# Optimization experiments

Measured on AMD Instinct MI355X. Metric: run time of the kernel, lower is better.

## Reference

```python
import jax, jax.numpy as jnp
import numpy as np


def setup_inputs() -> dict:
    key = jax.random.key(0)
    ka, kb = jax.random.split(key)
    B, S, I, J = 8, 8192, 256, 256
    a = jax.random.normal(ka, (B, S, I), dtype=jnp.float32)
    b = jax.random.normal(kb, (B, S, J), dtype=jnp.float32)
    return {"a": a, "b": b}


def reference(a, b):
    # mean_s(a_si outer b_sj) == (a^T @ b) / s, without materializing [*, i, j, s]
    s = a.shape[-2]
    out = jnp.einsum('...si,...sj->...ij', a, b) / s  # [*, i, j]
    return out
```

## Files before the change

kernel.cpp:

```cpp
#include <hip/hip_runtime.h>

typedef __bf16 bf16x8 __attribute__((ext_vector_type(8)));
typedef float f32x16 __attribute__((ext_vector_type(16)));
typedef float f32x4 __attribute__((ext_vector_type(4)));

#define S_TOTAL 8192
#define DIM 256
#define BK 16
#define NSP 16

__global__ __launch_bounds__(512, 4) void opm_partial(
    const float* __restrict__ A, const float* __restrict__ Bm,
    __bf16* __restrict__ dstbf, float* __restrict__ dstf32,
    int nsp, int kc, float scale)
{
    __shared__ float lA[3][BK * 256];
    __shared__ float lB[3][BK * 64];

    const int tid = threadIdx.x;
    const int w   = tid >> 6;
    const int l   = tid & 63;

    const int bid = blockIdx.x;
    const int x   = bid & 7;
    const int s   = bid >> 3;
    const int jq  = s & 3;
    const int gx  = s >> 2;
    const int g   = gx * 8 + x;
    const int batch = g / nsp;
    const int sp    = g % nsp;

    const long long base = (long long)batch * S_TOTAL * DIM;
    const int s0 = sp * kc;
    const int wr = w >> 1, wc = w & 1;
    const int lane31 = l & 31;
    const int hi = l >> 5;
    const int niter = kc / BK;

    f32x16 acc[2] = {};

    auto issue = [&](int it) {
        const int b3 = it % 3;
        const long long sb = (long long)(s0 + it * BK);
        __builtin_amdgcn_global_load_lds(
            (const __attribute__((address_space(1))) unsigned int*)(A + base + (sb + w) * DIM + 4 * l),
            (__attribute__((address_space(3))) unsigned int*)&lA[b3][w * 256], 16, 0, 0);
        __builtin_amdgcn_global_load_lds(
            (const __attribute__((address_space(1))) unsigned int*)(A + base + (sb + w + 8) * DIM + 4 * l),
            (__attribute__((address_space(3))) unsigned int*)&lA[b3][(w + 8) * 256], 16, 0, 0);
        if (w < 4) {
            __builtin_amdgcn_global_load_lds(
                (const __attribute__((address_space(1))) unsigned int*)(Bm + base + (sb + 4 * w + (l >> 4)) * DIM + jq * 64 + 4 * (l & 15)),
                (__attribute__((address_space(3))) unsigned int*)&lB[b3][4 * w * 64], 16, 0, 0);
        }
    };

    auto compute = [&](int b3) {
        const int i0 = wr * 64 + lane31;
        const int j0 = wc * 32 + lane31;
        bf16x8 af[2], bfv;
        #pragma unroll
        for (int mi = 0; mi < 2; ++mi)
            #pragma unroll
            for (int e = 0; e < 8; ++e)
                af[mi][e] = (__bf16)lA[b3][(hi * 8 + e) * 256 + i0 + mi * 32];
        #pragma unroll
        for (int e = 0; e < 8; ++e)
            bfv[e] = (__bf16)lB[b3][(hi * 8 + e) * 64 + j0];
        acc[0] = __builtin_amdgcn_mfma_f32_32x32x16_bf16(af[0], bfv, acc[0], 0, 0, 0);
        acc[1] = __builtin_amdgcn_mfma_f32_32x32x16_bf16(af[1], bfv, acc[1], 0, 0, 0);
    };

    issue(0);
    issue(1);

    for (int it = 0; it < niter; ++it) {
        const int rem = niter - 1 - it;
        if (w < 4) {
            if (rem >= 1) asm volatile("s_waitcnt vmcnt(3)" ::: "memory");
            else          asm volatile("s_waitcnt vmcnt(0)" ::: "memory");
        } else {
            if (rem >= 1) asm volatile("s_waitcnt vmcnt(2)" ::: "memory");
            else          asm volatile("s_waitcnt vmcnt(0)" ::: "memory");
        }
        __builtin_amdgcn_s_barrier();
        if (it + 2 < niter) issue(it + 2);
        compute(it % 3);
    }

    if (dstf32) {
        float* o = dstf32 + (long long)batch * (256 * 256) + jq * 64;
        #pragma unroll
        for (int mi = 0; mi < 2; ++mi)
        #pragma unroll
        for (int q = 0; q < 16; ++q) {
            const int row = (q & 3) + 8 * (q >> 2) + 4 * hi;
            const int i = wr * 64 + mi * 32 + row;
            const int j = wc * 32 + lane31;
            o[i * 256 + j] = acc[mi][q] * scale;
        }
    } else {
        __bf16* o = dstbf + (long long)((batch * nsp + sp) * 4 + jq) * 16384;
        __bf16* ebuf = (__bf16*)&lA[0][0];
        #pragma unroll
        for (int band = 0; band < 2; ++band) {
            __syncthreads();
            if ((wr >> 1) == band) {
                #pragma unroll
                for (int mi = 0; mi < 2; ++mi)
                #pragma unroll
                for (int q = 0; q < 16; ++q) {
                    const int lr = (wr & 1) * 64 + mi * 32 + (q & 3) + 8 * (q >> 2) + 4 * hi;
                    ebuf[lr * 64 + wc * 32 + lane31] = (__bf16)(acc[mi][q] * scale);
                }
            }
            __syncthreads();
            #pragma unroll
            for (int h = 0; h < 2; ++h) {
                const int G = tid + h * 512;
                *(bf16x8*)&o[band * 8192 + G * 8] = *(const bf16x8*)&ebuf[G * 8];
            }
        }
    }
}

__global__ __launch_bounds__(256) void opm_reduce16(
    const __bf16* __restrict__ ws, float* __restrict__ out)
{
    const int idx = blockIdx.x * 256 + threadIdx.x;
    const int batch = idx >> 13;
    const int gg  = idx & 8191;
    const int i   = gg >> 5;
    const int jgc = gg & 31;
    const int jq  = jgc >> 3;
    const int c8  = (jgc & 7) * 8;

    const bf16x8* p = (const bf16x8*)(ws + ((long long)(batch * NSP) * 4 + jq) * 16384 + i * 64 + c8);
    bf16x8 v[NSP];
    #pragma unroll
    for (int sp = 0; sp < NSP; ++sp) v[sp] = p[sp * 8192];

    float sacc[8] = {0.f, 0.f, 0.f, 0.f, 0.f, 0.f, 0.f, 0.f};
    #pragma unroll
    for (int sp = 0; sp < NSP; ++sp)
        #pragma unroll
        for (int e = 0; e < 8; ++e) sacc[e] += (float)v[sp][e];

    f32x4 lo = { sacc[0], sacc[1], sacc[2], sacc[3] };
    f32x4 hiv = { sacc[4], sacc[5], sacc[6], sacc[7] };
    lo  *= (1.0f / 8192.0f);
    hiv *= (1.0f / 8192.0f);
    ((f32x4*)out)[idx * 2]     = lo;
    ((f32x4*)out)[idx * 2 + 1] = hiv;
}

extern "C" void kernel_launch(void* const* d_in, const int* in_sizes, int n_in,
                              void* d_out, int out_size, void* d_ws, size_t ws_size,
                              hipStream_t stream)
{
    (void)in_sizes; (void)n_in; (void)out_size;
    const float* A  = (const float*)d_in[0];
    const float* Bm = (const float*)d_in[1];
    float* out = (float*)d_out;

    if (ws_size >= (size_t)8 * NSP * 4 * 16384 * sizeof(__bf16)) {
        opm_partial<<<32 * NSP, 512, 0, stream>>>(A, Bm, (__bf16*)d_ws, nullptr,
                                                  NSP, S_TOTAL / NSP, 1.0f);
        opm_reduce16<<<256, 256, 0, stream>>>((const __bf16*)d_ws, out);
    } else {
        opm_partial<<<32, 512, 0, stream>>>(A, Bm, nullptr, out, 1, S_TOTAL, 1.0f / 8192.0f);
    }
}
```

Before: 41.53 us.

## Switch partial GEMM tiles from 256x64 strips to 128x128 quadrants

Each block now computes a 128x128 quadrant of the output instead of a 256x64 column strip. It loads half of A's columns and half of B's columns per s-row, which cuts per-block global loads and removes redundant A reads across j-quarter blocks. Every wave now issues equal load counts, which simplifies the waitcnt logic, and LDS use shrinks. The workspace layout and reduce-kernel indexing are updated to match the quadrant ordering.

New measurement: 34.04 us. 1.22x faster.

```diff
diff --git a/kernel.cpp b/kernel.cpp
--- a/kernel.cpp
+++ b/kernel.cpp
@@ -14,25 +14,26 @@
     __bf16* __restrict__ dstbf, float* __restrict__ dstf32,
     int nsp, int kc, float scale)
 {
-    __shared__ float lA[3][BK * 256];
-    __shared__ float lB[3][BK * 64];
+    __shared__ float lds[3 * 4096];
 
     const int tid = threadIdx.x;
     const int w   = tid >> 6;
     const int l   = tid & 63;
 
-    const int bid = blockIdx.x;
-    const int x   = bid & 7;
-    const int s   = bid >> 3;
-    const int jq  = s & 3;
-    const int gx  = s >> 2;
-    const int g   = gx * 8 + x;
+    const int bid  = blockIdx.x;
+    const int x    = bid & 7;
+    const int r    = bid >> 3;
+    const int mate = r & 3;
+    const int gx   = r >> 2;
+    const int ih   = mate >> 1;
+    const int jh   = mate & 1;
+    const int g    = gx * 8 + x;
     const int batch = g / nsp;
     const int sp    = g % nsp;
 
     const long long base = (long long)batch * S_TOTAL * DIM;
     const int s0 = sp * kc;
-    const int wr = w >> 1, wc = w & 1;
+    const int wr = w >> 2, wc = w & 3;
     const int lane31 = l & 31;
     const int hi = l >> 5;
     const int niter = kc / BK;
@@ -40,33 +41,28 @@
     f32x16 acc[2] = {};
 
     auto issue = [&](int it) {
-        const int b3 = it % 3;
-        const long long sb = (long long)(s0 + it * BK);
+        float* buf = &lds[(it % 3) * 4096];
+        const long long srow = base + (long long)(s0 + it * BK + 2 * w + (l >> 5)) * DIM + 4 * (l & 31);
         __builtin_amdgcn_global_load_lds(
-            (const __attribute__((address_space(1))) unsigned int*)(A + base + (sb + w) * DIM + 4 * l),
-            (__attribute__((address_space(3))) unsigned int*)&lA[b3][w * 256], 16, 0, 0);
+            (const __attribute__((address_space(1))) unsigned int*)(A + srow + ih * 128),
+            (__attribute__((address_space(3))) unsigned int*)(buf + 2 * w * 128), 16, 0, 0);
         __builtin_amdgcn_global_load_lds(
-            (const __attribute__((address_space(1))) unsigned int*)(A + base + (sb + w + 8) * DIM + 4 * l),
-            (__attribute__((address_space(3))) unsigned int*)&lA[b3][(w + 8) * 256], 16, 0, 0);
-        if (w < 4) {
-            __builtin_amdgcn_global_load_lds(
-                (const __attribute__((address_space(1))) unsigned int*)(Bm + base + (sb + 4 * w + (l >> 4)) * DIM + jq * 64 + 4 * (l & 15)),
-                (__attribute__((address_space(3))) unsigned int*)&lB[b3][4 * w * 64], 16, 0, 0);
-        }
+            (const __attribute__((address_space(1))) unsigned int*)(Bm + srow + jh * 128),
+            (__attribute__((address_space(3))) unsigned int*)(buf + 2048 + 2 * w * 128), 16, 0, 0);
     };
 
     auto compute = [&](int b3) {
-        const int i0 = wr * 64 + lane31;
-        const int j0 = wc * 32 + lane31;
+        const float* bufA = &lds[b3 * 4096];
+        const float* bufB = bufA + 2048;
         bf16x8 af[2], bfv;
         #pragma unroll
         for (int mi = 0; mi < 2; ++mi)
             #pragma unroll
             for (int e = 0; e < 8; ++e)
-                af[mi][e] = (__bf16)lA[b3][(hi * 8 + e) * 256 + i0 + mi * 32];
+                af[mi][e] = (__bf16)bufA[(hi * 8 + e) * 128 + wr * 64 + mi * 32 + lane31];
         #pragma unroll
         for (int e = 0; e < 8; ++e)
-            bfv[e] = (__bf16)lB[b3][(hi * 8 + e) * 64 + j0];
+            bfv[e] = (__bf16)bufB[(hi * 8 + e) * 128 + wc * 32 + lane31];
         acc[0] = __builtin_amdgcn_mfma_f32_32x32x16_bf16(af[0], bfv, acc[0], 0, 0, 0);
         acc[1] = __builtin_amdgcn_mfma_f32_32x32x16_bf16(af[1], bfv, acc[1], 0, 0, 0);
     };
@@ -75,43 +71,35 @@
     issue(1);
 
     for (int it = 0; it < niter; ++it) {
-        const int rem = niter - 1 - it;
-        if (w < 4) {
-            if (rem >= 1) asm volatile("s_waitcnt vmcnt(3)" ::: "memory");
-            else          asm volatile("s_waitcnt vmcnt(0)" ::: "memory");
-        } else {
-            if (rem >= 1) asm volatile("s_waitcnt vmcnt(2)" ::: "memory");
-            else          asm volatile("s_waitcnt vmcnt(0)" ::: "memory");
-        }
+        if (it + 1 < niter) asm volatile("s_waitcnt vmcnt(2)" ::: "memory");
+        else                asm volatile("s_waitcnt vmcnt(0)" ::: "memory");
         __builtin_amdgcn_s_barrier();
         if (it + 2 < niter) issue(it + 2);
         compute(it % 3);
     }
 
     if (dstf32) {
-        float* o = dstf32 + (long long)batch * (256 * 256) + jq * 64;
+        float* o = dstf32 + (long long)batch * (256 * 256) + (ih * 128) * 256 + jh * 128;
         #pragma unroll
         for (int mi = 0; mi < 2; ++mi)
         #pragma unroll
         for (int q = 0; q < 16; ++q) {
             const int row = (q & 3) + 8 * (q >> 2) + 4 * hi;
-            const int i = wr * 64 + mi * 32 + row;
-            const int j = wc * 32 + lane31;
-            o[i * 256 + j] = acc[mi][q] * scale;
+            o[(wr * 64 + mi * 32 + row) * 256 + wc * 32 + lane31] = acc[mi][q] * scale;
         }
     } else {
-        __bf16* o = dstbf + (long long)((batch * nsp + sp) * 4 + jq) * 16384;
-        __bf16* ebuf = (__bf16*)&lA[0][0];
+        __bf16* o = dstbf + (long long)((batch * nsp + sp) * 4 + ih * 2 + jh) * 16384;
+        __bf16* ebuf = (__bf16*)&lds[0];
         #pragma unroll
         for (int band = 0; band < 2; ++band) {
             __syncthreads();
-            if ((wr >> 1) == band) {
+            if (wr == band) {
                 #pragma unroll
                 for (int mi = 0; mi < 2; ++mi)
                 #pragma unroll
                 for (int q = 0; q < 16; ++q) {
-                    const int lr = (wr & 1) * 64 + mi * 32 + (q & 3) + 8 * (q >> 2) + 4 * hi;
-                    ebuf[lr * 64 + wc * 32 + lane31] = (__bf16)(acc[mi][q] * scale);
+                    const int lr = mi * 32 + (q & 3) + 8 * (q >> 2) + 4 * hi;
+                    ebuf[lr * 128 + wc * 32 + lane31] = (__bf16)(acc[mi][q] * scale);
                 }
             }
             __syncthreads();
@@ -131,11 +119,12 @@
     const int batch = idx >> 13;
     const int gg  = idx & 8191;
     const int i   = gg >> 5;
-    const int jgc = gg & 31;
-    const int jq  = jgc >> 3;
-    const int c8  = (jgc & 7) * 8;
+    const int jg  = gg & 31;
+    const int ih  = i >> 7, ir = i & 127;
+    const int jh  = jg >> 4, jc = jg & 15;
 
-    const bf16x8* p = (const bf16x8*)(ws + ((long long)(batch * NSP) * 4 + jq) * 16384 + i * 64 + c8);
+    const bf16x8* p = (const bf16x8*)ws
+        + ((long long)(batch * NSP) * 4 + ih * 2 + jh) * 2048 + ir * 16 + jc;
     bf16x8 v[NSP];
     #pragma unroll
     for (int sp = 0; sp < NSP; ++sp) v[sp] = p[sp * 8192];
@@ -164,8 +153,8 @@
     float* out = (float*)d_out;
 
     if (ws_size >= (size_t)8 * NSP * 4 * 16384 * sizeof(__bf16)) {
-        opm_partial<<<32 * NSP, 512, 0, stream>>>(A, Bm, (__bf16*)d_ws, nullptr,
-                                                  NSP, S_TOTAL / NSP, 1.0f);
+        opm_partial<<<8 * NSP * 4, 512, 0, stream>>>(A, Bm, (__bf16*)d_ws, nullptr,
+                                                     NSP, S_TOTAL / NSP, 1.0f);
         opm_reduce16<<<256, 256, 0, stream>>>((const __bf16*)d_ws, out);
     } else {
         opm_partial<<<32, 512, 0, stream>>>(A, Bm, nullptr, out, 1, S_TOTAL, 1.0f / 8192.0f);
```
